# Kernel optimization log

Measured on AMD Instinct MI355X. Metric: run time of the kernel, lower is better.

The kernel has to match this reference:

```python
import jax, jax.numpy as jnp
import numpy as np

B, N, C, H, W = 32, 64, 3, 512, 512
P = 16               # patch_size
NUM_CLASSES = 128


def setup_inputs() -> dict:
    key = jax.random.key(0)
    k1, k2, k3, k4 = jax.random.split(key, 4)
    image = jax.random.normal(k1, (B, C, H, W), dtype=jnp.float32)
    emb = jax.random.normal(k2, (NUM_CLASSES, P * P * 3), dtype=jnp.float32)
    labels = jax.random.randint(k3, (B, N), 0, NUM_CLASSES)
    # precomputed top-left corners; original clamps so corners lie in [0, H-P]
    top_left = jax.random.randint(k4, (B, N, 2), 0, H - P + 1)
    return {"image": image, "emb": emb, "labels": labels, "top_left": top_left}


def reference(image, emb, labels, top_left):
    # gather patches: [B, N, 3, P, P]
    patches = emb[labels].reshape(B, N, 3, P, P)
    # reorder so channel dim trails the advanced-index result dims: [B, N, P, P, 3]
    vals = jnp.transpose(patches, (0, 1, 3, 4, 2))
    bb = jnp.arange(B)[:, None, None, None]                                 # [B,1,1,1]
    rr = top_left[..., 0][:, :, None, None] + jnp.arange(P)[None, None, :, None]  # [B,N,P,1]
    cc = top_left[..., 1][:, :, None, None] + jnp.arange(P)[None, None, None, :]  # [B,N,1,P]
    # scatter-add each patch into the image at its computed offset (overlaps sum)
    return image.at[bb, :, rr, cc].add(vals)
```

## Files before the change

### kernel.cpp

```cpp
#include <hip/hip_runtime.h>
#include <hip/hip_bf16.h>

#define B_   32
#define N_   64
#define C_   3
#define H_   512
#define W_   512
#define P_   16
#define PLANE (H_ * W_)
#define IMG   (C_ * PLANE)

typedef float f32x4 __attribute__((ext_vector_type(4)));

__global__ __launch_bounds__(256)
void ImagePatch_fused_kernel(const float* __restrict__ image,
                             const float* __restrict__ emb,
                             const int*   __restrict__ labels,
                             const int*   __restrict__ top_left,
                             float*       __restrict__ out) {
    __shared__ int s_cnt[2];
    __shared__ int s_dr[2][N_];
    __shared__ int s_tc[2][N_];
    __shared__ int s_lb[2][N_];

    const int bid = blockIdx.x;
    const int r0  = (bid & (H_ / 2 - 1)) * 2;
    const int b   = bid >> 8;
    const int tid = threadIdx.x;

    if (tid < 128) {
        const int w    = tid >> 6;
        const int lane = tid & 63;
        const int idx  = b * N_ + lane;
        const int tr   = top_left[idx * 2];
        const unsigned dr = (unsigned)(r0 + w - tr);
        const bool cover  = dr < P_;
        const unsigned long long m = __ballot(cover);
        if (cover) {
            const int pos = __popcll(m & ((1ull << lane) - 1ull));
            s_dr[w][pos] = (int)dr;
            s_tc[w][pos] = top_left[idx * 2 + 1];
            s_lb[w][pos] = labels[idx];
        }
        if (lane == 0) s_cnt[w] = __popcll(m);
    }
    __syncthreads();

    const int w  = tid >> 7;
    const int c0 = (tid & 127) * 4;
    const size_t base = (size_t)b * IMG + (size_t)(r0 + w) * W_ + c0;

    f32x4 v0 = __builtin_nontemporal_load((const f32x4*)(image + base));
    f32x4 v1 = __builtin_nontemporal_load((const f32x4*)(image + base + PLANE));
    f32x4 v2 = __builtin_nontemporal_load((const f32x4*)(image + base + 2 * PLANE));

    const int cnt = s_cnt[w];
    for (int k = 0; k < cnt; ++k) {
        const int tc = s_tc[w][k];
        if (c0 + 3 >= tc && c0 < tc + P_) {
            const float* e = emb + s_lb[w][k] * (C_ * P_ * P_) + s_dr[w][k] * P_;
            #pragma unroll
            for (int q = 0; q < 4; ++q) {
                const unsigned dc = (unsigned)(c0 + q - tc);
                if (dc < P_) {
                    v0[q] += e[dc];
                    v1[q] += e[P_ * P_ + dc];
                    v2[q] += e[2 * P_ * P_ + dc];
                }
            }
        }
    }

    __builtin_nontemporal_store(v0, (f32x4*)(out + base));
    __builtin_nontemporal_store(v1, (f32x4*)(out + base + PLANE));
    __builtin_nontemporal_store(v2, (f32x4*)(out + base + 2 * PLANE));
}

extern "C" void kernel_launch(void* const* d_in, const int* in_sizes, int n_in,
                              void* d_out, int out_size, void* d_ws, size_t ws_size,
                              hipStream_t stream) {
    const float* image    = (const float*)d_in[0];
    const float* emb      = (const float*)d_in[1];
    const int*   labels   = (const int*)d_in[2];
    const int*   top_left = (const int*)d_in[3];
    float*       out      = (float*)d_out;

    const int grid = B_ * H_ / 2;
    ImagePatch_fused_kernel<<<grid, 256, 0, stream>>>(image, emb, labels, top_left, out);
}
```

Before: 40.35 us.

## Replace shared-memory patch list with per-wave ballot and shuffle iteration

Each wavefront now handles half of one image row and loads all 64 patch descriptors itself. It packs row, column and label into one int and walks the covering patches with ballot, ffs and shfl. This removes the shared-memory compaction and the __syncthreads barrier. Nontemporal loads and stores are swapped for plain vector accesses, which changes cache behaviour on a purely streaming kernel. Every wave now redundantly loads the top_left and labels values.

After: 36.03 us. 1.12x faster.

```diff
diff --git a/kernel.cpp b/kernel.cpp
--- a/kernel.cpp
+++ b/kernel.cpp
@@ -18,50 +18,40 @@
                              const int*   __restrict__ labels,
                              const int*   __restrict__ top_left,
                              float*       __restrict__ out) {
-    __shared__ int s_cnt[2];
-    __shared__ int s_dr[2][N_];
-    __shared__ int s_tc[2][N_];
-    __shared__ int s_lb[2][N_];
+    const int tid  = threadIdx.x;
+    const int lane = tid & 63;
+    const int gw   = blockIdx.x * 4 + (tid >> 6);
+    const int half = gw & 1;
+    const int r    = (gw >> 1) & (H_ - 1);
+    const int b    = gw >> 10;
 
-    const int bid = blockIdx.x;
-    const int r0  = (bid & (H_ / 2 - 1)) * 2;
-    const int b   = bid >> 8;
-    const int tid = threadIdx.x;
+    const int idx = b * N_ + lane;
+    const int tr  = top_left[idx * 2];
+    const int tc  = top_left[idx * 2 + 1];
+    const int lb  = labels[idx];
+    const int pack = (tr << 16) | (tc << 7) | lb;
+    unsigned long long m = __ballot((unsigned)(r - tr) < P_);
 
-    if (tid < 128) {
-        const int w    = tid >> 6;
-        const int lane = tid & 63;
-        const int idx  = b * N_ + lane;
-        const int tr   = top_left[idx * 2];
-        const unsigned dr = (unsigned)(r0 + w - tr);
-        const bool cover  = dr < P_;
-        const unsigned long long m = __ballot(cover);
-        if (cover) {
-            const int pos = __popcll(m & ((1ull << lane) - 1ull));
-            s_dr[w][pos] = (int)dr;
-            s_tc[w][pos] = top_left[idx * 2 + 1];
-            s_lb[w][pos] = labels[idx];
-        }
-        if (lane == 0) s_cnt[w] = __popcll(m);
-    }
-    __syncthreads();
+    const int c0 = lane * 4 + half * 256;
+    const size_t base = (size_t)b * IMG + (size_t)r * W_ + c0;
 
-    const int w  = tid >> 7;
-    const int c0 = (tid & 127) * 4;
-    const size_t base = (size_t)b * IMG + (size_t)(r0 + w) * W_ + c0;
+    f32x4 v0 = *(const f32x4*)(image + base);
+    f32x4 v1 = *(const f32x4*)(image + base + PLANE);
+    f32x4 v2 = *(const f32x4*)(image + base + 2 * PLANE);
 
-    f32x4 v0 = __builtin_nontemporal_load((const f32x4*)(image + base));
-    f32x4 v1 = __builtin_nontemporal_load((const f32x4*)(image + base + PLANE));
-    f32x4 v2 = __builtin_nontemporal_load((const f32x4*)(image + base + 2 * PLANE));
-
-    const int cnt = s_cnt[w];
-    for (int k = 0; k < cnt; ++k) {
-        const int tc = s_tc[w][k];
-        if (c0 + 3 >= tc && c0 < tc + P_) {
-            const float* e = emb + s_lb[w][k] * (C_ * P_ * P_) + s_dr[w][k] * P_;
+    while (m) {
+        const int k = __ffsll((unsigned long long)m) - 1;
+        m &= m - 1;
+        const int pk   = __shfl(pack, k);
+        const int tr_k = pk >> 16;
+        const int tc_k = (pk >> 7) & 0x1FF;
+        const int lb_k = pk & 0x7F;
+        const int dr   = r - tr_k;
+        if (c0 + 3 >= tc_k && c0 < tc_k + P_) {
+            const float* e = emb + lb_k * (C_ * P_ * P_) + dr * P_;
             #pragma unroll
             for (int q = 0; q < 4; ++q) {
-                const unsigned dc = (unsigned)(c0 + q - tc);
+                const unsigned dc = (unsigned)(c0 + q - tc_k);
                 if (dc < P_) {
                     v0[q] += e[dc];
                     v1[q] += e[P_ * P_ + dc];
@@ -71,9 +61,9 @@
         }
     }
 
-    __builtin_nontemporal_store(v0, (f32x4*)(out + base));
-    __builtin_nontemporal_store(v1, (f32x4*)(out + base + PLANE));
-    __builtin_nontemporal_store(v2, (f32x4*)(out + base + 2 * PLANE));
+    *(f32x4*)(out + base)             = v0;
+    *(f32x4*)(out + base + PLANE)     = v1;
+    *(f32x4*)(out + base + 2 * PLANE) = v2;
 }
 
 extern "C" void kernel_launch(void* const* d_in, const int* in_sizes, int n_in,
@@ -85,6 +75,6 @@
     const int*   top_left = (const int*)d_in[3];
     float*       out      = (float*)d_out;
 
-    const int grid = B_ * H_ / 2;
+    const int grid = B_ * H_ * 2 / 4;
     ImagePatch_fused_kernel<<<grid, 256, 0, stream>>>(image, emb, labels, top_left, out);
 }
```
